# Kernel optimization log

Hardware: AMD Instinct MI355X
Metric: run time of the kernel (lower is better)

Reference implementation:

```python
import jax, jax.numpy as jnp
import numpy as np

B, S, H = 2, 2048, 1024
NUM_HEADS = 16


def setup_inputs() -> dict:
    key = jax.random.key(0)
    ks = jax.random.split(key, 5)
    scale = 1.0 / np.sqrt(H)
    x = jax.random.normal(ks[0], (B, S, H), dtype=jnp.float32)
    W_qkv = jax.random.normal(ks[1], (3 * H, H), dtype=jnp.float32) * scale
    b_qkv = jax.random.normal(ks[2], (3 * H,), dtype=jnp.float32) * 0.02
    W_o = jax.random.normal(ks[3], (H, H), dtype=jnp.float32) * scale
    b_o = jax.random.normal(ks[4], (H,), dtype=jnp.float32) * 0.02
    return {"x": x, "W_qkv": W_qkv, "b_qkv": b_qkv, "W_o": W_o, "b_o": b_o}


def reference(x, W_qkv, b_qkv, W_o, b_o):
    b, s, h = x.shape
    n = NUM_HEADS
    d_head = h // n
    # QKV projection (torch Linear: x @ W.T + b), then chunk into Q, K, V
    qkv = x @ W_qkv.T + b_qkv                      # [b, s, 3h]
    Q, K, V = jnp.split(qkv, 3, axis=-1)           # each [b, s, h]
    # split heads: b s (n d) -> b n s d
    Q = Q.reshape(b, s, n, d_head).transpose(0, 2, 1, 3)
    K = K.reshape(b, s, n, d_head).transpose(0, 2, 1, 3)
    V = V.reshape(b, s, n, d_head).transpose(0, 2, 1, 3)
    # scores, causal mask, scale (mask before/after scale is equivalent: -inf stays -inf)
    scores = jnp.einsum('bnqd,bnkd->bnqk', Q, K) / jnp.sqrt(jnp.float32(d_head))
    causal = jnp.tril(jnp.ones((s, s), dtype=bool))  # True = keep
    scores = jnp.where(causal, scores, -jnp.inf)
    A = jax.nn.softmax(scores, axis=-1)
    AV = jnp.einsum('bnqk,bnkd->bnqd', A, V)
    out = AV.transpose(0, 2, 1, 3).reshape(b, s, h)  # merge heads
    return out @ W_o.T + b_o
```

## Files before the change

### kernel.cpp

```cpp
#include <hip/hip_runtime.h>
#include <cstdint>
#include <cstddef>

#define BATCH 2
#define SEQ   2048
#define HID   1024
#define NHEAD 16
#define DHEAD 64
#define QKV_N 3072
#define NTOK  4096

typedef __attribute__((ext_vector_type(4))) float f32x4;
typedef __attribute__((ext_vector_type(8))) short bf16x8;

#define QSCL 0.18033688011112042f

__device__ inline unsigned short f2bf(float f) {
    union { float f; unsigned int u; } v; v.f = f;
    unsigned int u = v.u;
    unsigned int r = (u + 0x7fffu + ((u >> 16) & 1u)) >> 16;
    return (unsigned short)r;
}

__device__ __forceinline__ void gload_lds16(const void* g, void* l) {
    __builtin_amdgcn_global_load_lds(
        (const __attribute__((address_space(1))) void*)g,
        (__attribute__((address_space(3))) void*)l, 16, 0, 0);
}

__global__ void cast_f32_bf16(const float* __restrict__ in, unsigned short* __restrict__ out, int n4) {
    int i = blockIdx.x * blockDim.x + threadIdx.x;
    if (i >= n4) return;
    float4 v = reinterpret_cast<const float4*>(in)[i];
    ushort4 o;
    o.x = f2bf(v.x); o.y = f2bf(v.y); o.z = f2bf(v.z); o.w = f2bf(v.w);
    reinterpret_cast<ushort4*>(out)[i] = o;
}

template<int BN, int OUT_MODE>
__global__ __launch_bounds__(256) void gemm_bt(const short* __restrict__ A,
                                               const short* __restrict__ B,
                                               const float* __restrict__ bias,
                                               void* __restrict__ Cout,
                                               int M, int N, int K) {
    constexpr int WTN = BN / 2;
    constexpr int NJ  = WTN / 16;
    constexpr int NBC = BN / 64;

    __shared__ short sA[2][128 * 32];
    __shared__ short sB[2][BN * 32];

    const int tid  = threadIdx.x;
    const int lane = tid & 63;
    const int wave = tid >> 6;
    const int wm = wave >> 1, wn = wave & 1;

    const int nwg = gridDim.x;
    const int swz = (blockIdx.x & 7) * (nwg >> 3) + (blockIdx.x >> 3);
    const int tiles_n = N / BN;
    const int m0 = (swz / tiles_n) * 128;
    const int n0 = (swz % tiles_n) * BN;

    f32x4 acc[4][NJ];
    #pragma unroll
    for (int i = 0; i < 4; ++i)
        #pragma unroll
        for (int j = 0; j < NJ; ++j) acc[i][j] = (f32x4){0.f, 0.f, 0.f, 0.f};

    const int r = lane & 15;
    const int G = lane >> 4;

    #define GSTAGE(kt_, buf_)                                                          \
        {                                                                              \
            _Pragma("unroll")                                                          \
            for (int i = 0; i < 2; ++i) {                                              \
                int ga = (i * 4 + wave) * 64 + lane;                                   \
                int row = ga >> 2, gcol = (ga & 3) ^ (row & 3);                        \
                gload_lds16(A + (size_t)(m0 + row) * K + (kt_) + gcol * 8,             \
                            &sA[buf_][(i * 4 + wave) * 512]);                          \
            }                                                                          \
            _Pragma("unroll")                                                          \
            for (int i = 0; i < NBC; ++i) {                                            \
                int gb = (i * 4 + wave) * 64 + lane;                                   \
                int row = gb >> 2, gcol = (gb & 3) ^ (row & 3);                        \
                gload_lds16(B + (size_t)(n0 + row) * K + (kt_) + gcol * 8,             \
                            &sB[buf_][(i * 4 + wave) * 512]);                          \
            }                                                                          \
        }

    GSTAGE(0, 0);
    __syncthreads();
    int cur = 0;

    const int nsteps = K >> 5;
    for (int ks = 0; ks < nsteps; ++ks) {
        if (ks + 1 < nsteps) GSTAGE((ks + 1) * 32, cur ^ 1);

        const int sg = G ^ (r & 3);
        bf16x8 af[4], bfr[NJ];
        #pragma unroll
        for (int i = 0; i < 4; ++i) {
            int row = wm * 64 + i * 16 + r;
            af[i] = *reinterpret_cast<const bf16x8*>(&sA[cur][row * 32 + sg * 8]);
        }
        #pragma unroll
        for (int j = 0; j < NJ; ++j) {
            int row = wn * WTN + j * 16 + r;
            bfr[j] = *reinterpret_cast<const bf16x8*>(&sB[cur][row * 32 + sg * 8]);
        }
        #pragma unroll
        for (int i = 0; i < 4; ++i)
            #pragma unroll
            for (int j = 0; j < NJ; ++j)
                acc[i][j] = __builtin_amdgcn_mfma_f32_16x16x32_bf16(af[i], bfr[j], acc[i][j], 0, 0, 0);

        __syncthreads();
        cur ^= 1;
    }
    #undef GSTAGE

    const int col_l = lane & 15;
    const int row_g = (lane >> 4) * 4;
    #pragma unroll
    for (int i = 0; i < 4; ++i) {
        #pragma unroll
        for (int j = 0; j < NJ; ++j) {
            int nn = n0 + wn * WTN + j * 16 + col_l;
            float bv = bias[nn];
            float scl = (OUT_MODE == 2 && nn < HID) ? QSCL : 1.0f;
            #pragma unroll
            for (int reg = 0; reg < 4; ++reg) {
                int mm = m0 + wm * 64 + i * 16 + row_g + reg;
                float v = (acc[i][j][reg] + bv) * scl;
                if (OUT_MODE == 0) {
                    reinterpret_cast<float*>(Cout)[(size_t)mm * N + nn] = v;
                } else {
                    reinterpret_cast<unsigned short*>(Cout)[(size_t)mm * N + nn] = f2bf(v);
                }
            }
        }
    }
}

#define TLDP 72
__global__ __launch_bounds__(256) void transpose_v(const short* __restrict__ qkv,
                                                   short* __restrict__ vT) {
    const int st = blockIdx.x;
    const int bh = blockIdx.y;
    const int b  = bh >> 4, h = bh & 15;
    __shared__ short ld[64 * TLDP];
    const int tid = threadIdx.x;

    #pragma unroll
    for (int i = 0; i < 2; ++i) {
        int idx = i * 256 + tid;
        int row = idx >> 3, c = idx & 7;
        int4 v = *reinterpret_cast<const int4*>(
            qkv + ((size_t)(b * SEQ + st * 64 + row)) * QKV_N + 2 * HID + h * DHEAD + c * 8);
        *reinterpret_cast<int4*>(&ld[row * TLDP + c * 8]) = v;
    }
    __syncthreads();
    #pragma unroll
    for (int i = 0; i < 4; ++i) {
        int idx = i * 256 + tid;
        int d = idx >> 4, sc = idx & 15;
        ushort4 o;
        o.x = (unsigned short)ld[(sc * 4 + 0) * TLDP + d];
        o.y = (unsigned short)ld[(sc * 4 + 1) * TLDP + d];
        o.z = (unsigned short)ld[(sc * 4 + 2) * TLDP + d];
        o.w = (unsigned short)ld[(sc * 4 + 3) * TLDP + d];
        *reinterpret_cast<ushort4*>(&vT[((size_t)(bh * DHEAD + d)) * SEQ + st * 64 + sc * 4]) = o;
    }
}

#define SWZ(g_, row_) ((g_) ^ ((row_) & 7))

__global__ __launch_bounds__(128, 2) void attn_fwd(const short* __restrict__ qkv,
                                                   const short* __restrict__ vT,
                                                   short* __restrict__ av) {
    const int bh = blockIdx.y;
    const int b  = bh >> 4;
    const int h  = bh & 15;
    const int qt = (31 - blockIdx.x + blockIdx.y) & 31;

    __shared__ short sK [2][64 * 64];
    __shared__ short sVT[2][64 * 64];

    const int tid  = threadIdx.x;
    const int lane = tid & 63;
    const int wave = tid >> 6;
    const int r    = lane & 15;
    const int G    = lane >> 4;
    const int row_g = G * 4;

    const int qbw = qt * 64 + wave * 32;

    bf16x8 qf[2][2];
    #pragma unroll
    for (int mi = 0; mi < 2; ++mi) {
        const short* Qg = qkv + ((size_t)(b * SEQ + qbw + mi * 16 + r)) * QKV_N + h * DHEAD;
        qf[mi][0] = *reinterpret_cast<const bf16x8*>(Qg + G * 8);
        qf[mi][1] = *reinterpret_cast<const bf16x8*>(Qg + 32 + G * 8);
    }

    f32x4 oacc[2][4];
    f32x4 oL[2];
    #pragma unroll
    for (int mi = 0; mi < 2; ++mi) {
        oL[mi] = (f32x4){0.f, 0.f, 0.f, 0.f};
        #pragma unroll
        for (int dg = 0; dg < 4; ++dg) oacc[mi][dg] = (f32x4){0.f, 0.f, 0.f, 0.f};
    }

    bf16x8 ones;
    #pragma unroll
    for (int e = 0; e < 8; ++e) ones[e] = (short)0x3f80;

    const int lrow = lane >> 3;
    const int lsg  = lane & 7;

    #define STAGE(kv0_, buf_)                                                              \
        {                                                                                  \
            _Pragma("unroll")                                                              \
            for (int i = 0; i < 4; ++i) {                                                  \
                int row  = i * 16 + wave * 8 + lrow;                                       \
                int srcg = lsg ^ (row & 7);                                                \
                gload_lds16(qkv + (size_t)(b * SEQ + (kv0_) + row) * QKV_N                 \
                                + HID + h * DHEAD + srcg * 8,                              \
                            &sK[buf_][(i * 128 + wave * 64) * 8]);                         \
                gload_lds16(vT + (size_t)(bh * DHEAD + row) * SEQ + (kv0_) + srcg * 8,     \
                            &sVT[buf_][(i * 128 + wave * 64) * 8]);                        \
            }                                                                              \
        }

    STAGE(0, 0);
    __syncthreads();
    int cur = 0;

    for (int t = 0; t <= qt; ++t) {
        if (t < qt) STAGE((t + 1) * 64, cur ^ 1);

        bf16x8 kb[4][2];
        #pragma unroll
        for (int g = 0; g < 4; ++g) {
            int row = g * 16 + r;
            kb[g][0] = *reinterpret_cast<const bf16x8*>(&sK[cur][row * 64 + SWZ(G, row) * 8]);
            kb[g][1] = *reinterpret_cast<const bf16x8*>(&sK[cur][row * 64 + SWZ(4 + G, row) * 8]);
        }
        bf16x8 vb[4][2];
        #pragma unroll
        for (int dg = 0; dg < 4; ++dg) {
            int row_d = dg * 16 + r;
            int rm = row_d & 7;
            int eo = (G & 1) * 4;
            #pragma unroll
            for (int c = 0; c < 2; ++c) {
                int glo = (c * 4 + (G >> 1)) ^ rm;
                int ghi = (c * 4 + 2 + (G >> 1)) ^ rm;
                uint2 lo = *reinterpret_cast<const uint2*>(&sVT[cur][row_d * 64 + glo * 8 + eo]);
                uint2 hi = *reinterpret_cast<const uint2*>(&sVT[cur][row_d * 64 + ghi * 8 + eo]);
                int4 f; f.x = lo.x; f.y = lo.y; f.z = hi.x; f.w = hi.y;
                __builtin_memcpy(&vb[dg][c], &f, 16);
            }
        }

        const bool diag = (t == qt);

        #pragma unroll
        for (int mi = 0; mi < 2; ++mi) {
            f32x4 s[4];
            #pragma unroll
            for (int g = 0; g < 4; ++g) {
                f32x4 z = (f32x4){0.f, 0.f, 0.f, 0.f};
                z = __builtin_amdgcn_mfma_f32_16x16x32_bf16(kb[g][0], qf[mi][0], z, 0, 0, 0);
                z = __builtin_amdgcn_mfma_f32_16x16x32_bf16(kb[g][1], qf[mi][1], z, 0, 0, 0);
                s[g] = z;
            }
            if (diag) {
                int qg = wave * 32 + mi * 16 + r;
                #pragma unroll
                for (int g = 0; g < 4; ++g) {
                    #pragma unroll
                    for (int reg = 0; reg < 4; ++reg) {
                        int kvg = g * 16 + row_g + reg;
                        if (kvg > qg) s[g][reg] = -30000.f;
                    }
                }
            }
            bf16x8 pb[2];
            #pragma unroll
            for (int c = 0; c < 2; ++c) {
                unsigned int w[4];
                #pragma unroll
                for (int hh = 0; hh < 2; ++hh) {
                    float p0 = __builtin_amdgcn_exp2f(s[2 * c + hh][0]);
                    float p1 = __builtin_amdgcn_exp2f(s[2 * c + hh][1]);
                    float p2 = __builtin_amdgcn_exp2f(s[2 * c + hh][2]);
                    float p3 = __builtin_amdgcn_exp2f(s[2 * c + hh][3]);
                    w[hh * 2 + 0] = (unsigned int)f2bf(p0) | ((unsigned int)f2bf(p1) << 16);
                    w[hh * 2 + 1] = (unsigned int)f2bf(p2) | ((unsigned int)f2bf(p3) << 16);
                }
                int4 f; f.x = (int)w[0]; f.y = (int)w[1]; f.z = (int)w[2]; f.w = (int)w[3];
                __builtin_memcpy(&pb[c], &f, 16);
            }

            #pragma unroll
            for (int dg = 0; dg < 4; ++dg) {
                oacc[mi][dg] = __builtin_amdgcn_mfma_f32_16x16x32_bf16(vb[dg][0], pb[0], oacc[mi][dg], 0, 0, 0);
                oacc[mi][dg] = __builtin_amdgcn_mfma_f32_16x16x32_bf16(vb[dg][1], pb[1], oacc[mi][dg], 0, 0, 0);
            }
            oL[mi] = __builtin_amdgcn_mfma_f32_16x16x32_bf16(ones, pb[0], oL[mi], 0, 0, 0);
            oL[mi] = __builtin_amdgcn_mfma_f32_16x16x32_bf16(ones, pb[1], oL[mi], 0, 0, 0);
        }

        __syncthreads();
        cur ^= 1;
    }

    #pragma unroll
    for (int mi = 0; mi < 2; ++mi) {
        float il = 1.0f / oL[mi][0];
        size_t tok = (size_t)(b * SEQ + qbw + mi * 16 + r);
        #pragma unroll
        for (int dg = 0; dg < 4; ++dg) {
            ushort4 o;
            o.x = f2bf(oacc[mi][dg][0] * il);
            o.y = f2bf(oacc[mi][dg][1] * il);
            o.z = f2bf(oacc[mi][dg][2] * il);
            o.w = f2bf(oacc[mi][dg][3] * il);
            *reinterpret_cast<ushort4*>(&av[tok * HID + h * DHEAD + dg * 16 + row_g]) = o;
        }
    }
}

extern "C" void kernel_launch(void* const* d_in, const int* in_sizes, int n_in,
                              void* d_out, int out_size, void* d_ws, size_t ws_size,
                              hipStream_t stream) {
    const float* x     = (const float*)d_in[0];
    const float* W_qkv = (const float*)d_in[1];
    const float* b_qkv = (const float*)d_in[2];
    const float* W_o   = (const float*)d_in[3];
    const float* b_o   = (const float*)d_in[4];
    float* out = (float*)d_out;

    const int n_x    = NTOK * HID;
    const int n_wqkv = QKV_N * HID;
    const int n_wo   = HID * HID;
    const int n_qkv  = NTOK * QKV_N;
    const int n_av   = NTOK * HID;

    short* xb    = (short*)d_ws;
    short* wqkvb = xb + n_x;
    short* wob   = wqkvb + n_wqkv;
    short* qkv   = wob + n_wo;
    short* av    = qkv + n_qkv;
    short* vT    = av + n_av;

    cast_f32_bf16<<<n_x / 1024,    256, 0, stream>>>(x,     (unsigned short*)xb,    n_x / 4);
    cast_f32_bf16<<<n_wqkv / 1024, 256, 0, stream>>>(W_qkv, (unsigned short*)wqkvb, n_wqkv / 4);
    cast_f32_bf16<<<n_wo / 1024,   256, 0, stream>>>(W_o,   (unsigned short*)wob,   n_wo / 4);

    gemm_bt<128, 2><<<(NTOK / 128) * (QKV_N / 128), 256, 0, stream>>>(
        xb, wqkvb, b_qkv, (void*)qkv, NTOK, QKV_N, HID);

    transpose_v<<<dim3(SEQ / 64, BATCH * NHEAD), 256, 0, stream>>>(qkv, vT);

    attn_fwd<<<dim3(32, 32), 128, 0, stream>>>(qkv, vT, av);

    gemm_bt<64, 0><<<(NTOK / 128) * (HID / 64), 256, 0, stream>>>(
        av, wob, b_o, (void*)out, NTOK, HID, HID);
}
```

Measured before the change: 131.1 us.

## Restructure attention into single-wave blocks with 32-row tiles and waitcnt pipelining

The attention kernel now launches 2048 single-wave blocks, each covering 32 query rows and stepping over 32-key tiles, where before 1024 two-wave blocks covered 64 query rows and stepped over 64-key tiles. Because each block is one wave, __syncthreads is replaced with explicit s_waitcnt vmcnt waits on the async global-to-LDS loads plus a sched_barrier. The V swizzle is adapted to the narrower tile. The aim is finer causal load balance, no block-level barriers, and more blocks to fill the GPU. The cost is twice as many loop iterations per key length, smaller MFMA batches per iteration, and reliance on a hand-counted vmcnt and on single-wave LDS ordering being correct.

```diff
diff --git a/kernel.cpp b/kernel.cpp
--- a/kernel.cpp
+++ b/kernel.cpp
@@ -173,27 +173,24 @@
     }
 }
 
-#define SWZ(g_, row_) ((g_) ^ ((row_) & 7))
-
-__global__ __launch_bounds__(128, 2) void attn_fwd(const short* __restrict__ qkv,
-                                                   const short* __restrict__ vT,
-                                                   short* __restrict__ av) {
-    const int bh = blockIdx.y;
-    const int b  = bh >> 4;
-    const int h  = bh & 15;
-    const int qt = (31 - blockIdx.x + blockIdx.y) & 31;
-
-    __shared__ short sK [2][64 * 64];
-    __shared__ short sVT[2][64 * 64];
-
-    const int tid  = threadIdx.x;
-    const int lane = tid & 63;
-    const int wave = tid >> 6;
+__global__ __launch_bounds__(64, 2) void attn_fwd(const short* __restrict__ qkv,
+                                                  const short* __restrict__ vT,
+                                                  short* __restrict__ av) {
+    const int bid = blockIdx.x;
+    const int qb  = 63 - (bid >> 5);
+    const int bh  = bid & 31;
+    const int b   = bh >> 4;
+    const int h   = bh & 15;
+
+    __shared__ short sK [2][32 * 64];
+    __shared__ short sVT[2][64 * 32];
+
+    const int lane = threadIdx.x;
     const int r    = lane & 15;
     const int G    = lane >> 4;
     const int row_g = G * 4;
 
-    const int qbw = qt * 64 + wave * 32;
+    const int qbw = qb * 32;
 
     bf16x8 qf[2][2];
     #pragma unroll
@@ -216,104 +213,109 @@
     #pragma unroll
     for (int e = 0; e < 8; ++e) ones[e] = (short)0x3f80;
 
-    const int lrow = lane >> 3;
-    const int lsg  = lane & 7;
+    const int krow_ = lane >> 3, kgr_ = lane & 7;
+    const int vrow_ = lane >> 2, vgr_ = lane & 3;
 
     #define STAGE(kv0_, buf_)                                                              \
         {                                                                                  \
             _Pragma("unroll")                                                              \
             for (int i = 0; i < 4; ++i) {                                                  \
-                int row  = i * 16 + wave * 8 + lrow;                                       \
-                int srcg = lsg ^ (row & 7);                                                \
+                int row  = i * 8 + krow_;                                                  \
+                int srcg = kgr_ ^ (row & 7);                                               \
                 gload_lds16(qkv + (size_t)(b * SEQ + (kv0_) + row) * QKV_N                 \
                                 + HID + h * DHEAD + srcg * 8,                              \
-                            &sK[buf_][(i * 128 + wave * 64) * 8]);                         \
+                            &sK[buf_][i * 512]);                                           \
+            }                                                                              \
+            _Pragma("unroll")                                                              \
+            for (int i = 0; i < 4; ++i) {                                                  \
+                int row  = i * 16 + vrow_;                                                 \
+                int srcg = vgr_ ^ (row & 3);                                               \
                 gload_lds16(vT + (size_t)(bh * DHEAD + row) * SEQ + (kv0_) + srcg * 8,     \
-                            &sVT[buf_][(i * 128 + wave * 64) * 8]);                        \
+                            &sVT[buf_][i * 512]);                                          \
             }                                                                              \
         }
 
     STAGE(0, 0);
-    __syncthreads();
     int cur = 0;
 
-    for (int t = 0; t <= qt; ++t) {
-        if (t < qt) STAGE((t + 1) * 64, cur ^ 1);
-
-        bf16x8 kb[4][2];
-        #pragma unroll
-        for (int g = 0; g < 4; ++g) {
+    for (int t = 0; t <= qb; ++t) {
+        if (t < qb) {
+            STAGE((t + 1) * 32, cur ^ 1);
+            asm volatile("s_waitcnt vmcnt(8)" ::: "memory");
+        } else {
+            asm volatile("s_waitcnt vmcnt(0)" ::: "memory");
+        }
+        __builtin_amdgcn_sched_barrier(0);
+
+        bf16x8 kb[2][2];
+        #pragma unroll
+        for (int g = 0; g < 2; ++g) {
             int row = g * 16 + r;
-            kb[g][0] = *reinterpret_cast<const bf16x8*>(&sK[cur][row * 64 + SWZ(G, row) * 8]);
-            kb[g][1] = *reinterpret_cast<const bf16x8*>(&sK[cur][row * 64 + SWZ(4 + G, row) * 8]);
-        }
-        bf16x8 vb[4][2];
+            kb[g][0] = *reinterpret_cast<const bf16x8*>(&sK[cur][row * 64 + ((0 + G) ^ (row & 7)) * 8]);
+            kb[g][1] = *reinterpret_cast<const bf16x8*>(&sK[cur][row * 64 + ((4 + G) ^ (row & 7)) * 8]);
+        }
+        bf16x8 vb[4];
         #pragma unroll
         for (int dg = 0; dg < 4; ++dg) {
             int row_d = dg * 16 + r;
-            int rm = row_d & 7;
+            int rm = row_d & 3;
             int eo = (G & 1) * 4;
+            int glo = (G >> 1) ^ rm;
+            int ghi = (2 + (G >> 1)) ^ rm;
+            uint2 lo = *reinterpret_cast<const uint2*>(&sVT[cur][row_d * 32 + glo * 8 + eo]);
+            uint2 hi = *reinterpret_cast<const uint2*>(&sVT[cur][row_d * 32 + ghi * 8 + eo]);
+            int4 f; f.x = lo.x; f.y = lo.y; f.z = hi.x; f.w = hi.y;
+            __builtin_memcpy(&vb[dg], &f, 16);
+        }
+
+        const bool diag = (t == qb);
+
+        #pragma unroll
+        for (int mi = 0; mi < 2; ++mi) {
+            f32x4 s[2];
             #pragma unroll
-            for (int c = 0; c < 2; ++c) {
-                int glo = (c * 4 + (G >> 1)) ^ rm;
-                int ghi = (c * 4 + 2 + (G >> 1)) ^ rm;
-                uint2 lo = *reinterpret_cast<const uint2*>(&sVT[cur][row_d * 64 + glo * 8 + eo]);
-                uint2 hi = *reinterpret_cast<const uint2*>(&sVT[cur][row_d * 64 + ghi * 8 + eo]);
-                int4 f; f.x = lo.x; f.y = lo.y; f.z = hi.x; f.w = hi.y;
-                __builtin_memcpy(&vb[dg][c], &f, 16);
-            }
-        }
-
-        const bool diag = (t == qt);
-
-        #pragma unroll
-        for (int mi = 0; mi < 2; ++mi) {
-            f32x4 s[4];
-            #pragma unroll
-            for (int g = 0; g < 4; ++g) {
+            for (int g = 0; g < 2; ++g) {
                 f32x4 z = (f32x4){0.f, 0.f, 0.f, 0.f};
                 z = __builtin_amdgcn_mfma_f32_16x16x32_bf16(kb[g][0], qf[mi][0], z, 0, 0, 0);
                 z = __builtin_amdgcn_mfma_f32_16x16x32_bf16(kb[g][1], qf[mi][1], z, 0, 0, 0);
                 s[g] = z;
             }
             if (diag) {
-                int qg = wave * 32 + mi * 16 + r;
+                int ql = mi * 16 + r;
                 #pragma unroll
-                for (int g = 0; g < 4; ++g) {
+                for (int g = 0; g < 2; ++g) {
                     #pragma unroll
                     for (int reg = 0; reg < 4; ++reg) {
-                        int kvg = g * 16 + row_g + reg;
-                        if (kvg > qg) s[g][reg] = -30000.f;
+                        int kvl = g * 16 + row_g + reg;
+                        if (kvl > ql) s[g][reg] = -30000.f;
                     }
                 }
             }
-            bf16x8 pb[2];
+            unsigned int w0, w1, w2, w3;
+            {
+                float p0 = __builtin_amdgcn_exp2f(s[0][0]);
+                float p1 = __builtin_amdgcn_exp2f(s[0][1]);
+                float p2 = __builtin_amdgcn_exp2f(s[0][2]);
+                float p3 = __builtin_amdgcn_exp2f(s[0][3]);
+                float p4 = __builtin_amdgcn_exp2f(s[1][0]);
+                float p5 = __builtin_amdgcn_exp2f(s[1][1]);
+                float p6 = __builtin_amdgcn_exp2f(s[1][2]);
+                float p7 = __builtin_amdgcn_exp2f(s[1][3]);
+                w0 = (unsigned int)f2bf(p0) | ((unsigned int)f2bf(p1) << 16);
+                w1 = (unsigned int)f2bf(p2) | ((unsigned int)f2bf(p3) << 16);
+                w2 = (unsigned int)f2bf(p4) | ((unsigned int)f2bf(p5) << 16);
+                w3 = (unsigned int)f2bf(p6) | ((unsigned int)f2bf(p7) << 16);
+            }
+            bf16x8 pb;
+            { int4 f; f.x = (int)w0; f.y = (int)w1; f.z = (int)w2; f.w = (int)w3;
+              __builtin_memcpy(&pb, &f, 16); }
+
             #pragma unroll
-            for (int c = 0; c < 2; ++c) {
-                unsigned int w[4];
-                #pragma unroll
-                for (int hh = 0; hh < 2; ++hh) {
-                    float p0 = __builtin_amdgcn_exp2f(s[2 * c + hh][0]);
-                    float p1 = __builtin_amdgcn_exp2f(s[2 * c + hh][1]);
-                    float p2 = __builtin_amdgcn_exp2f(s[2 * c + hh][2]);
-                    float p3 = __builtin_amdgcn_exp2f(s[2 * c + hh][3]);
-                    w[hh * 2 + 0] = (unsigned int)f2bf(p0) | ((unsigned int)f2bf(p1) << 16);
-                    w[hh * 2 + 1] = (unsigned int)f2bf(p2) | ((unsigned int)f2bf(p3) << 16);
-                }
-                int4 f; f.x = (int)w[0]; f.y = (int)w[1]; f.z = (int)w[2]; f.w = (int)w[3];
-                __builtin_memcpy(&pb[c], &f, 16);
-            }
-
-            #pragma unroll
-            for (int dg = 0; dg < 4; ++dg) {
-                oacc[mi][dg] = __builtin_amdgcn_mfma_f32_16x16x32_bf16(vb[dg][0], pb[0], oacc[mi][dg], 0, 0, 0);
-                oacc[mi][dg] = __builtin_amdgcn_mfma_f32_16x16x32_bf16(vb[dg][1], pb[1], oacc[mi][dg], 0, 0, 0);
-            }
-            oL[mi] = __builtin_amdgcn_mfma_f32_16x16x32_bf16(ones, pb[0], oL[mi], 0, 0, 0);
-            oL[mi] = __builtin_amdgcn_mfma_f32_16x16x32_bf16(ones, pb[1], oL[mi], 0, 0, 0);
-        }
-
-        __syncthreads();
+            for (int dg = 0; dg < 4; ++dg)
+                oacc[mi][dg] = __builtin_amdgcn_mfma_f32_16x16x32_bf16(vb[dg], pb, oacc[mi][dg], 0, 0, 0);
+            oL[mi] = __builtin_amdgcn_mfma_f32_16x16x32_bf16(ones, pb, oL[mi], 0, 0, 0);
+        }
+
         cur ^= 1;
     }
 
@@ -365,7 +367,7 @@
 
     transpose_v<<<dim3(SEQ / 64, BATCH * NHEAD), 256, 0, stream>>>(qkv, vT);
 
-    attn_fwd<<<dim3(32, 32), 128, 0, stream>>>(qkv, vT, av);
+    attn_fwd<<<2048, 64, 0, stream>>>(qkv, vT, av);
 
     gemm_bt<64, 0><<<(NTOK / 128) * (HID / 64), 256, 0, stream>>>(
         av, wob, b_o, (void*)out, NTOK, HID, HID);
```

Measured after the change: 129.4 us. No clear change (-1.3%).
